# Optimization experiments

Measured on AMD Instinct MI355X. Metric: run time of the kernel, lower is better.

The kernel has to match this reference:

```python
import jax, jax.numpy as jnp
import numpy as np

B, N, E, D, AD = 2, 4096, 4, 64, 32


def setup_inputs() -> dict:
    key = jax.random.key(0)
    ks = jax.random.split(key, 10)
    s = 0.02  # init std matching module _initialization
    return {
        "prop_state": jax.random.normal(ks[0], (B, N, D), jnp.float32),
        "annotation": jax.random.normal(ks[1], (B, N, AD), jnp.float32),
        "A": jax.random.uniform(ks[2], (B, N, N * E), jnp.float32),
        "W_in": jax.random.normal(ks[3], (E, D, D), jnp.float32) * s,
        "b_in": jnp.zeros((E, D), jnp.float32),
        "Wr": jax.random.normal(ks[4], (D, 2 * D), jnp.float32) * s,
        "br": jnp.zeros((D,), jnp.float32),
        "Wz": jax.random.normal(ks[5], (D, 2 * D), jnp.float32) * s,
        "bz": jnp.zeros((D,), jnp.float32),
        "Wh": jax.random.normal(ks[6], (D, 2 * D), jnp.float32) * s,
        "bh": jnp.zeros((D,), jnp.float32),
        "Wo1": jax.random.normal(ks[7], (D, D + AD), jnp.float32) * s,
        "bo1": jnp.zeros((D,), jnp.float32),
        "Wo2": jax.random.normal(ks[8], (1, D), jnp.float32) * s,
        "bo2": jnp.zeros((1,), jnp.float32),
    }


def reference(prop_state, annotation, A, W_in, b_in, Wr, br, Wz, bz, Wh, bh, Wo1, bo1, Wo2, bo2):
    b, n, d = prop_state.shape
    e = W_in.shape[0]
    # per-edge-type input transforms: [B, E, N, D] -> [B, E*N, D] (edge-type major)
    in_states = jnp.einsum('bnd,eod->beno', prop_state, W_in) + b_in[None, :, None, :]
    in_flat = in_states.reshape(b, e * n, d)
    # dense adjacency aggregation: A [B, N, N*E] x in_flat [B, N*E, D]
    a_in = jnp.einsum('bnm,bmd->bnd', A, in_flat)
    # GRU-style gated node update
    a = jnp.concatenate([a_in, prop_state], axis=-1)  # [B, N, 2D]
    r = jax.nn.sigmoid(a @ Wr.T + br)
    z = jax.nn.sigmoid(a @ Wz.T + bz)
    h_hat = jnp.tanh(jnp.concatenate([a_in, r * prop_state], axis=-1) @ Wh.T + bh)
    new_state = (1.0 - z) * prop_state + z * h_hat  # [B, N, D]
    # output head
    join = jnp.concatenate([new_state, annotation], axis=-1)  # [B, N, D+AD]
    h = jnp.tanh(join @ Wo1.T + bo1)
    out = (h @ Wo2.T + bo2).sum(axis=2)  # [B, N]
    return out
```

## Files before the change

### kernel.cpp

```cpp
#include <hip/hip_runtime.h>
#include <hip/hip_bf16.h>
#include <stdint.h>

typedef __bf16 bf16x8 __attribute__((ext_vector_type(8)));
typedef float  f32x16 __attribute__((ext_vector_type(16)));
typedef float  f32x4  __attribute__((ext_vector_type(4)));

static constexpr int Bz = 2, Nn = 4096, Ee = 4, Dd = 64, ADim = 32;
static constexpr int Mm = Nn * Ee;
static constexpr int KSEG = 8;
static constexpr int KLEN = Mm / KSEG;
static constexpr int NT = Bz * Nn / 32;
static constexpr int PHK = 256;
static constexpr int NPH = KLEN / PHK;

__device__ __forceinline__ bf16x8 cvt8(float4 a, float4 b) {
  bf16x8 r;
  r[0] = (__bf16)a.x; r[1] = (__bf16)a.y; r[2] = (__bf16)a.z; r[3] = (__bf16)a.w;
  r[4] = (__bf16)b.x; r[5] = (__bf16)b.y; r[6] = (__bf16)b.z; r[7] = (__bf16)b.w;
  return r;
}
__device__ __forceinline__ bf16x8 cvt8v(f32x4 a, f32x4 b) {
  bf16x8 r;
  r[0] = (__bf16)a[0]; r[1] = (__bf16)a[1]; r[2] = (__bf16)a[2]; r[3] = (__bf16)a[3];
  r[4] = (__bf16)b[0]; r[5] = (__bf16)b[1]; r[6] = (__bf16)b[2]; r[7] = (__bf16)b[3];
  return r;
}
__device__ __forceinline__ f32x16 zero16() {
  f32x16 z;
#pragma unroll
  for (int i = 0; i < 16; ++i) z[i] = 0.f;
  return z;
}
__device__ __forceinline__ f32x16 mm(bf16x8 a, bf16x8 b, f32x16 c) {
  return __builtin_amdgcn_mfma_f32_32x32x16_bf16(a, b, c, 0, 0, 0);
}
__device__ __forceinline__ float sigm(float x) { return 1.f / (1.f + __expf(-x)); }
__device__ __forceinline__ float tanh_fast(float x) {
  float e = __expf(2.f * x);
  return 1.f - 2.f / (e + 1.f);
}
__device__ __forceinline__ void async_lds16(const void* g, void* l) {
  __builtin_amdgcn_global_load_lds(
      (const __attribute__((address_space(1))) uint32_t*)g,
      (__attribute__((address_space(3))) uint32_t*)l, 16, 0, 0);
}

__global__ __launch_bounds__(256) void k_packbt(
    const float* __restrict__ prop, const float* __restrict__ Win,
    const float* __restrict__ bin, __bf16* __restrict__ Bt,
    const float* __restrict__ Wr, const float* __restrict__ Wz,
    const float* __restrict__ Wh, const float* __restrict__ Wo1,
    __bf16* __restrict__ Wp) {
  const int bid = blockIdx.x;
  const int tid = threadIdx.x;
  const int w = tid >> 6, l = tid & 63;
  const int r31 = l & 31, h = l >> 5;

  if (bid == 512) {
    for (int f = w; f < 60; f += 4) {
      const float* W; int L, fl;
      if (f < 16)      { W = Wr;  L = 128; fl = f; }
      else if (f < 32) { W = Wz;  L = 128; fl = f - 16; }
      else if (f < 48) { W = Wh;  L = 128; fl = f - 32; }
      else             { W = Wo1; L = 96;  fl = f - 48; }
      const int ks = fl >> 1, oh = fl & 1;
      const float* src = W + (size_t)(32 * oh + r31) * L + 16 * ks + 8 * h;
      float4 s0 = *reinterpret_cast<const float4*>(src);
      float4 s1 = *reinterpret_cast<const float4*>(src + 4);
      *reinterpret_cast<bf16x8*>(Wp + ((size_t)f * 64 + l) * 8) = cvt8(s0, s1);
    }
    return;
  }
  const int nchunk = bid & 63;
  const int e = (bid >> 6) & 3, b = bid >> 8;
  const int oh = w & 1, ns = w >> 1;
  const int o_row = oh * 32 + r31;
  const int n_col = nchunk * 64 + ns * 32 + r31;
  const float* wbase = Win + ((size_t)e * 64 + o_row) * 64 + 8 * h;
  const float* pbase = prop + ((size_t)b * Nn + n_col) * 64 + 8 * h;
  f32x16 acc = zero16();
#pragma unroll
  for (int ks = 0; ks < 4; ++ks) {
    float4 w0 = *reinterpret_cast<const float4*>(wbase + 16 * ks);
    float4 w1 = *reinterpret_cast<const float4*>(wbase + 16 * ks + 4);
    float4 p0 = *reinterpret_cast<const float4*>(pbase + 16 * ks);
    float4 p1 = *reinterpret_cast<const float4*>(pbase + 16 * ks + 4);
    acc = mm(cvt8(w0, w1), cvt8(p0, p1), acc);
  }
#pragma unroll
  for (int reg = 0; reg < 16; ++reg) {
    int orow = oh * 32 + (reg & 3) + 8 * (reg >> 2) + 4 * h;
    float v = acc[reg] + bin[e * 64 + orow];
    Bt[((size_t)b * 64 + orow) * Mm + (size_t)e * Nn + n_col] = (__bf16)v;
  }
}

__global__ __launch_bounds__(512, 1) void k_big_gemm(
    const float* __restrict__ A, const __bf16* __restrict__ Bt,
    __bf16* __restrict__ part) {
  __shared__ float  ahalf[2][64][PHK];
  __shared__ __bf16 btl[64][PHK];

  const int bid = blockIdx.x;
  const int kseg = bid & 7;
  const int tg   = bid >> 3;
  const int bb   = tg >> 4;
  const int gg   = tg & 15;
  const int ph0  = tg & (NPH - 1);
  const int tid = threadIdx.x;
  const int w = tid >> 6, l = tid & 63;
  const int r31 = l & 31, h = l >> 5;
  const int tp = w >> 2, q = (w >> 1) & 1, kh = w & 1;

  const size_t kbase = (size_t)kseg * KLEN;
  const float*  Ab  = A  + ((size_t)bb * Nn + gg * 256) * Mm + kbase;
  const __bf16* BtB = Bt + (size_t)bb * 64 * Mm + kbase;

#define ISSUE_A(pi, pr, hf)                                                  \
  { _Pragma("unroll")                                                        \
    for (int j_ = 0; j_ < 8; ++j_) {                                         \
      const int rw_ = 8 * w + j_;                                            \
      const float* src_ = Ab + (size_t)((pi) * 64 + rw_) * Mm +              \
                          (size_t)(pr) * PHK + ((l ^ (rw_ & 7)) << 2);       \
      async_lds16(src_, (void*)&ahalf[hf][rw_][0]);                          \
    } }

  bf16x8 btreg[4];
  const int btrh = l >> 5;
  const int btu  = l & 31;
#define LOAD_BT(pr)                                                          \
  { _Pragma("unroll")                                                        \
    for (int j_ = 0; j_ < 4; ++j_) {                                         \
      const int row_ = 8 * w + 2 * j_ + btrh;                                \
      btreg[j_] = *reinterpret_cast<const bf16x8*>(                          \
          BtB + (size_t)row_ * Mm + (size_t)(pr) * PHK + btu * 8);           \
    } }
#define WRITE_BT                                                             \
  { _Pragma("unroll")                                                        \
    for (int j_ = 0; j_ < 4; ++j_) {                                         \
      const int row_ = 8 * w + 2 * j_ + btrh;                                \
      *reinterpret_cast<bf16x8*>(&btl[row_][(btu ^ (row_ & 7)) * 8]) =       \
          btreg[j_];                                                         \
    } }

  const int swz  = r31 & 7;
  const int arow = tp * 32 + r31;
  const int brow = 32 * q + r31;
  f32x16 acc[4] = {zero16(), zero16(), zero16(), zero16()};

#define COMPUTE(pi, hf)                                                      \
  { _Pragma("unroll")                                                        \
    for (int s_ = 0; s_ < 8; ++s_) {                                         \
      const int ua_ = kh * 32 + 4 * s_ + 2 * h;                              \
      f32x4 fa0 = *reinterpret_cast<const f32x4*>(                           \
          &ahalf[hf][arow][((ua_ ^ swz) << 2)]);                             \
      f32x4 fa1 = *reinterpret_cast<const f32x4*>(                           \
          &ahalf[hf][arow][(((ua_ + 1) ^ swz) << 2)]);                       \
      const int ub_ = kh * 16 + 2 * s_ + h;                                  \
      bf16x8 fb = *reinterpret_cast<const bf16x8*>(                          \
          &btl[brow][((ub_ ^ swz) * 8)]);                                    \
      acc[pi] = mm(cvt8v(fa0, fa1), fb, acc[pi]);                            \
    } }

  LOAD_BT(ph0);
  ISSUE_A(0, ph0, 0);
  ISSUE_A(1, ph0, 1);
  asm volatile("s_waitcnt vmcnt(16)" ::: "memory");
  WRITE_BT;
  asm volatile("s_waitcnt vmcnt(8) lgkmcnt(0)" ::: "memory");
  __builtin_amdgcn_s_barrier();

  for (int pp = 0; pp < NPH; ++pp) {
    const bool lastp = (pp == NPH - 1);
    const int prc = (pp + ph0) & (NPH - 1);
    const int prn = (pp + 1 + ph0) & (NPH - 1);
    COMPUTE(0, 0);
    __builtin_amdgcn_s_barrier();
    ISSUE_A(2, prc, 0);
    asm volatile("s_waitcnt vmcnt(8)" ::: "memory");
    __builtin_amdgcn_s_barrier();
    COMPUTE(1, 1);
    __builtin_amdgcn_s_barrier();
    if (!lastp) LOAD_BT(prn);
    ISSUE_A(3, prc, 1);
    asm volatile("s_waitcnt vmcnt(8)" ::: "memory");
    __builtin_amdgcn_s_barrier();
    COMPUTE(2, 0);
    __builtin_amdgcn_s_barrier();
    if (!lastp) {
      ISSUE_A(0, prn, 0);
      asm volatile("s_waitcnt vmcnt(8)" ::: "memory");
    } else {
      asm volatile("s_waitcnt vmcnt(0)" ::: "memory");
    }
    __builtin_amdgcn_s_barrier();
    COMPUTE(3, 1);
    if (!lastp) {
      __builtin_amdgcn_s_barrier();
      WRITE_BT;
      ISSUE_A(1, prn, 1);
      asm volatile("s_waitcnt vmcnt(8) lgkmcnt(0)" ::: "memory");
      __builtin_amdgcn_s_barrier();
    }
  }
#undef ISSUE_A
#undef LOAD_BT
#undef WRITE_BT
#undef COMPUTE

  float* scratch = &ahalf[0][0][0];
  if (kh == 1) {
#pragma unroll
    for (int i = 0; i < 4; ++i) {
      float* slot = scratch + (size_t)(i * 4 + tp * 2 + q) * 1024 + l * 16;
#pragma unroll
      for (int r = 0; r < 16; r += 4) {
        f32x4 v; v[0] = acc[i][r]; v[1] = acc[i][r + 1];
        v[2] = acc[i][r + 2]; v[3] = acc[i][r + 3];
        *reinterpret_cast<f32x4*>(slot + r) = v;
      }
    }
  }
  __syncthreads();
  if (kh == 0) {
#pragma unroll
    for (int i = 0; i < 4; ++i) {
      const int tile = bb * 128 + gg * 8 + i * 2 + tp;
      __bf16* pb = part + ((size_t)tile * KSEG + kseg) * 2048 + 32 * q;
      const float* slot = scratch + (size_t)(i * 4 + tp * 2 + q) * 1024 + l * 16;
#pragma unroll
      for (int reg = 0; reg < 16; ++reg) {
        int row = (reg & 3) + 8 * (reg >> 2) + 4 * h;
        pb[row * 64 + r31] = (__bf16)(acc[i][reg] + slot[reg]);
      }
    }
  }
}

__global__ __launch_bounds__(128) void k_gru(
    const __bf16* __restrict__ part, const float* __restrict__ prop,
    const float* __restrict__ annot, const __bf16* __restrict__ Wp,
    const float* __restrict__ br, const float* __restrict__ bz,
    const float* __restrict__ bh, const float* __restrict__ bo1,
    const float* __restrict__ Wo2, const float* __restrict__ bo2,
    float* __restrict__ out) {
  __shared__ float plds[32][68];
  __shared__ float tlds[32][68];
  __shared__ float sred[32];
  const int tile = blockIdx.x;
  const int R0 = tile * 32;
  const int tid = threadIdx.x;
  const int wv = tid >> 6;
  const int l = tid & 63;
  const int r31 = l & 31, h = l >> 5;

  bf16x8 xa[4], xp[4], xan[2];
  {
    const __bf16* pt = part + (size_t)tile * (KSEG * 2048) + (size_t)r31 * 64 + 8 * h;
    const float* pb = prop + (size_t)(R0 + r31) * 64 + 8 * h;
#pragma unroll
    for (int ks = 0; ks < 4; ++ks) {
      float s[8] = {0.f, 0.f, 0.f, 0.f, 0.f, 0.f, 0.f, 0.f};
#pragma unroll
      for (int seg = 0; seg < KSEG; ++seg) {
        bf16x8 v = *reinterpret_cast<const bf16x8*>(pt + seg * 2048 + 16 * ks);
#pragma unroll
        for (int j = 0; j < 8; ++j) s[j] += (float)v[j];
      }
      bf16x8 x;
#pragma unroll
      for (int j = 0; j < 8; ++j) x[j] = (__bf16)s[j];
      xa[ks] = x;
      float4 p0 = *reinterpret_cast<const float4*>(pb + 16 * ks);
      float4 p1 = *reinterpret_cast<const float4*>(pb + 16 * ks + 4);
      xp[ks] = cvt8(p0, p1);
      if (wv == 0) {
        *reinterpret_cast<float4*>(&plds[r31][16 * ks + 8 * h]) = p0;
        *reinterpret_cast<float4*>(&plds[r31][16 * ks + 8 * h + 4]) = p1;
      }
    }
    const float* anb = annot + (size_t)(R0 + r31) * ADim + 8 * h;
#pragma unroll
    for (int ks = 0; ks < 2; ++ks) {
      float4 a0 = *reinterpret_cast<const float4*>(anb + 16 * ks);
      float4 a1 = *reinterpret_cast<const float4*>(anb + 16 * ks + 4);
      xan[ks] = cvt8(a0, a1);
    }
  }
  __syncthreads();

#define LDWP(base, ks, oh) \
  (*reinterpret_cast<const bf16x8*>(Wp + (((size_t)(base) + (ks) * 2 + (oh)) * 64 + l) * 8))

  f32x16 aR = zero16(), aZ = zero16();
#pragma unroll
  for (int ks = 0; ks < 8; ++ks) {
    bf16x8 af = (ks < 4) ? xa[ks] : xp[ks - 4];
    aR = mm(af, LDWP(0, ks, wv), aR);
    aZ = mm(af, LDWP(16, ks, wv), aZ);
  }
  const float br_ = br[32 * wv + r31];
  const float bz_ = bz[32 * wv + r31];
  float propv[16], zv[16];
  const int oc = 32 * wv + r31;
#pragma unroll
  for (int reg = 0; reg < 16; ++reg) {
    int row = (reg & 3) + 8 * (reg >> 2) + 4 * h;
    propv[reg] = plds[row][oc];
    float rv = sigm(aR[reg] + br_);
    zv[reg] = sigm(aZ[reg] + bz_);
    tlds[row][oc] = rv * propv[reg];
  }
  __syncthreads();
  bf16x8 xr[4];
#pragma unroll
  for (int ks = 0; ks < 4; ++ks) {
    float4 t0 = *reinterpret_cast<const float4*>(&tlds[r31][16 * ks + 8 * h]);
    float4 t1 = *reinterpret_cast<const float4*>(&tlds[r31][16 * ks + 8 * h + 4]);
    xr[ks] = cvt8(t0, t1);
  }
  f32x16 aH = zero16();
#pragma unroll
  for (int ks = 0; ks < 8; ++ks) {
    bf16x8 af = (ks < 4) ? xa[ks] : xr[ks - 4];
    aH = mm(af, LDWP(32, ks, wv), aH);
  }
  __syncthreads();
  const float bh_ = bh[32 * wv + r31];
#pragma unroll
  for (int reg = 0; reg < 16; ++reg) {
    int row = (reg & 3) + 8 * (reg >> 2) + 4 * h;
    float hh = tanh_fast(aH[reg] + bh_);
    float z = zv[reg];
    tlds[row][oc] = (1.f - z) * propv[reg] + z * hh;
  }
  __syncthreads();
  bf16x8 xn[4];
#pragma unroll
  for (int ks = 0; ks < 4; ++ks) {
    float4 t0 = *reinterpret_cast<const float4*>(&tlds[r31][16 * ks + 8 * h]);
    float4 t1 = *reinterpret_cast<const float4*>(&tlds[r31][16 * ks + 8 * h + 4]);
    xn[ks] = cvt8(t0, t1);
  }
  f32x16 aO = zero16();
#pragma unroll
  for (int ks = 0; ks < 6; ++ks) {
    bf16x8 af = (ks < 4) ? xn[ks] : xan[ks - 4];
    aO = mm(af, LDWP(48, ks, wv), aO);
  }
  const float bo1_ = bo1[32 * wv + r31];
  const float wo2_ = Wo2[32 * wv + r31];
  const float bo2v = bo2[0];
  float pred[16];
#pragma unroll
  for (int reg = 0; reg < 16; ++reg) {
    float p = tanh_fast(aO[reg] + bo1_) * wo2_;
#pragma unroll
    for (int mks = 16; mks >= 1; mks >>= 1) p += __shfl_xor(p, mks, 64);
    pred[reg] = p;
  }
  if (wv == 1 && r31 == 0) {
#pragma unroll
    for (int reg = 0; reg < 16; ++reg) sred[reg * 2 + h] = pred[reg];
  }
  __syncthreads();
  if (wv == 0 && r31 == 0) {
#pragma unroll
    for (int reg = 0; reg < 16; ++reg) {
      int row = (reg & 3) + 8 * (reg >> 2) + 4 * h;
      out[R0 + row] = pred[reg] + sred[reg * 2 + h] + bo2v;
    }
  }
#undef LDWP
}

extern "C" void kernel_launch(void* const* d_in, const int* in_sizes, int n_in,
                              void* d_out, int out_size, void* d_ws, size_t ws_size,
                              hipStream_t stream) {
  const float* prop  = (const float*)d_in[0];
  const float* annot = (const float*)d_in[1];
  const float* A     = (const float*)d_in[2];
  const float* Win   = (const float*)d_in[3];
  const float* bin   = (const float*)d_in[4];
  const float* Wr    = (const float*)d_in[5];
  const float* br    = (const float*)d_in[6];
  const float* Wz    = (const float*)d_in[7];
  const float* bz    = (const float*)d_in[8];
  const float* Wh    = (const float*)d_in[9];
  const float* bh    = (const float*)d_in[10];
  const float* Wo1   = (const float*)d_in[11];
  const float* bo1   = (const float*)d_in[12];
  const float* Wo2   = (const float*)d_in[13];
  const float* bo2   = (const float*)d_in[14];
  float* out = (float*)d_out;

  char* ws = (char*)d_ws;
  __bf16* Bt   = (__bf16*)ws;
  __bf16* part = (__bf16*)(ws + (size_t)4 * 1024 * 1024);
  __bf16* Wp   = (__bf16*)(ws + (size_t)16 * 1024 * 1024);

  k_packbt<<<dim3(513), 256, 0, stream>>>(prop, Win, bin, Bt,
                                          Wr, Wz, Wh, Wo1, Wp);
  k_big_gemm<<<dim3(256), 512, 0, stream>>>(A, Bt, part);
  k_gru<<<dim3(NT), 128, 0, stream>>>(part, prop, annot, Wp,
                                      br, bz, bh, bo1, Wo2, bo2, out);
}
```

Before: 127.8 us.

## Fuse pack, big GEMM and GRU kernels into one cooperative kernel

Merges the three launches (B-transpose pack, split-K adjacency GEMM, GRU/output head) into a single cooperative kernel of 256 blocks separated by grid-wide syncs. Shared memory is unioned between the GEMM and GRU phases, and the pack work is remapped so each 512-thread block covers two of the old 256-thread blocks. The aim is to remove the launch gaps and tail effects between kernels. The cost is two grid barriers, and in the GRU phase only 2 of 8 waves do work, leaving 256 blocks of mostly idle threads.

```diff
diff --git a/kernel.cpp b/kernel.cpp
--- a/kernel.cpp
+++ b/kernel.cpp
@@ -1,6 +1,9 @@
 #include <hip/hip_runtime.h>
 #include <hip/hip_bf16.h>
+#include <hip/hip_cooperative_groups.h>
 #include <stdint.h>
+
+namespace cg = cooperative_groups;
 
 typedef __bf16 bf16x8 __attribute__((ext_vector_type(8)));
 typedef float  f32x16 __attribute__((ext_vector_type(16)));
@@ -46,76 +49,82 @@
       (__attribute__((address_space(3))) uint32_t*)l, 16, 0, 0);
 }
 
-__global__ __launch_bounds__(256) void k_packbt(
-    const float* __restrict__ prop, const float* __restrict__ Win,
-    const float* __restrict__ bin, __bf16* __restrict__ Bt,
-    const float* __restrict__ Wr, const float* __restrict__ Wz,
-    const float* __restrict__ Wh, const float* __restrict__ Wo1,
-    __bf16* __restrict__ Wp) {
+__global__ __launch_bounds__(512, 1) void k_fused(
+    const float* __restrict__ prop, const float* __restrict__ annot,
+    const float* __restrict__ A, const float* __restrict__ Win,
+    const float* __restrict__ bin,
+    const float* __restrict__ Wr, const float* __restrict__ br,
+    const float* __restrict__ Wz, const float* __restrict__ bz,
+    const float* __restrict__ Wh, const float* __restrict__ bh,
+    const float* __restrict__ Wo1, const float* __restrict__ bo1,
+    const float* __restrict__ Wo2, const float* __restrict__ bo2,
+    __bf16* __restrict__ Bt, __bf16* __restrict__ part,
+    __bf16* __restrict__ Wp, float* __restrict__ out) {
+  __shared__ union {
+    struct { float ahalf[2][64][PHK]; __bf16 btl[64][PHK]; } g;
+    struct { float plds[32][68]; float tlds[32][68]; float sred[32]; } r;
+  } smem;
+
+  cg::grid_group grid = cg::this_grid();
   const int bid = blockIdx.x;
   const int tid = threadIdx.x;
   const int w = tid >> 6, l = tid & 63;
   const int r31 = l & 31, h = l >> 5;
 
-  if (bid == 512) {
-    for (int f = w; f < 60; f += 4) {
-      const float* W; int L, fl;
-      if (f < 16)      { W = Wr;  L = 128; fl = f; }
-      else if (f < 32) { W = Wz;  L = 128; fl = f - 16; }
-      else if (f < 48) { W = Wh;  L = 128; fl = f - 32; }
-      else             { W = Wo1; L = 96;  fl = f - 48; }
-      const int ks = fl >> 1, oh = fl & 1;
-      const float* src = W + (size_t)(32 * oh + r31) * L + 16 * ks + 8 * h;
-      float4 s0 = *reinterpret_cast<const float4*>(src);
-      float4 s1 = *reinterpret_cast<const float4*>(src + 4);
-      *reinterpret_cast<bf16x8*>(Wp + ((size_t)f * 64 + l) * 8) = cvt8(s0, s1);
-    }
-    return;
+  {
+    const int sub = 2 * bid + (w >> 2);
+    const int wsub = w & 3;
+    const int nchunk = sub & 63;
+    const int e = (sub >> 6) & 3, b = sub >> 8;
+    const int oh = wsub & 1, ns = wsub >> 1;
+    const int o_row = oh * 32 + r31;
+    const int n_col = nchunk * 64 + ns * 32 + r31;
+    const float* wbase = Win + ((size_t)e * 64 + o_row) * 64 + 8 * h;
+    const float* pbase = prop + ((size_t)b * Nn + n_col) * 64 + 8 * h;
+    f32x16 acc = zero16();
+#pragma unroll
+    for (int ks = 0; ks < 4; ++ks) {
+      float4 w0 = *reinterpret_cast<const float4*>(wbase + 16 * ks);
+      float4 w1 = *reinterpret_cast<const float4*>(wbase + 16 * ks + 4);
+      float4 p0 = *reinterpret_cast<const float4*>(pbase + 16 * ks);
+      float4 p1 = *reinterpret_cast<const float4*>(pbase + 16 * ks + 4);
+      acc = mm(cvt8(w0, w1), cvt8(p0, p1), acc);
+    }
+#pragma unroll
+    for (int reg = 0; reg < 16; ++reg) {
+      int orow = oh * 32 + (reg & 3) + 8 * (reg >> 2) + 4 * h;
+      float v = acc[reg] + bin[e * 64 + orow];
+      Bt[((size_t)b * 64 + orow) * Mm + (size_t)e * Nn + n_col] = (__bf16)v;
+    }
+    if (bid == 0) {
+      for (int f = w; f < 60; f += 8) {
+        const float* W; int L, fl;
+        if (f < 16)      { W = Wr;  L = 128; fl = f; }
+        else if (f < 32) { W = Wz;  L = 128; fl = f - 16; }
+        else if (f < 48) { W = Wh;  L = 128; fl = f - 32; }
+        else             { W = Wo1; L = 96;  fl = f - 48; }
+        const int ks = fl >> 1, oh2 = fl & 1;
+        const float* src = W + (size_t)(32 * oh2 + r31) * L + 16 * ks + 8 * h;
+        float4 s0 = *reinterpret_cast<const float4*>(src);
+        float4 s1 = *reinterpret_cast<const float4*>(src + 4);
+        *reinterpret_cast<bf16x8*>(Wp + ((size_t)f * 64 + l) * 8) = cvt8(s0, s1);
+      }
+    }
   }
-  const int nchunk = bid & 63;
-  const int e = (bid >> 6) & 3, b = bid >> 8;
-  const int oh = w & 1, ns = w >> 1;
-  const int o_row = oh * 32 + r31;
-  const int n_col = nchunk * 64 + ns * 32 + r31;
-  const float* wbase = Win + ((size_t)e * 64 + o_row) * 64 + 8 * h;
-  const float* pbase = prop + ((size_t)b * Nn + n_col) * 64 + 8 * h;
-  f32x16 acc = zero16();
-#pragma unroll
-  for (int ks = 0; ks < 4; ++ks) {
-    float4 w0 = *reinterpret_cast<const float4*>(wbase + 16 * ks);
-    float4 w1 = *reinterpret_cast<const float4*>(wbase + 16 * ks + 4);
-    float4 p0 = *reinterpret_cast<const float4*>(pbase + 16 * ks);
-    float4 p1 = *reinterpret_cast<const float4*>(pbase + 16 * ks + 4);
-    acc = mm(cvt8(w0, w1), cvt8(p0, p1), acc);
-  }
-#pragma unroll
-  for (int reg = 0; reg < 16; ++reg) {
-    int orow = oh * 32 + (reg & 3) + 8 * (reg >> 2) + 4 * h;
-    float v = acc[reg] + bin[e * 64 + orow];
-    Bt[((size_t)b * 64 + orow) * Mm + (size_t)e * Nn + n_col] = (__bf16)v;
-  }
-}
-
-__global__ __launch_bounds__(512, 1) void k_big_gemm(
-    const float* __restrict__ A, const __bf16* __restrict__ Bt,
-    __bf16* __restrict__ part) {
-  __shared__ float  ahalf[2][64][PHK];
-  __shared__ __bf16 btl[64][PHK];
-
-  const int bid = blockIdx.x;
-  const int kseg = bid & 7;
-  const int tg   = bid >> 3;
-  const int bb   = tg >> 4;
-  const int gg   = tg & 15;
-  const int ph0  = tg & (NPH - 1);
-  const int tid = threadIdx.x;
-  const int w = tid >> 6, l = tid & 63;
-  const int r31 = l & 31, h = l >> 5;
-  const int tp = w >> 2, q = (w >> 1) & 1, kh = w & 1;
-
-  const size_t kbase = (size_t)kseg * KLEN;
-  const float*  Ab  = A  + ((size_t)bb * Nn + gg * 256) * Mm + kbase;
-  const __bf16* BtB = Bt + (size_t)bb * 64 * Mm + kbase;
+  __threadfence();
+  grid.sync();
+
+  {
+    const int kseg = bid & 7;
+    const int tg   = bid >> 3;
+    const int bb   = tg >> 4;
+    const int gg   = tg & 15;
+    const int ph0  = tg & (NPH - 1);
+    const int tp = w >> 2, q = (w >> 1) & 1, kh = w & 1;
+
+    const size_t kbase = (size_t)kseg * KLEN;
+    const float*  Ab  = A  + ((size_t)bb * Nn + gg * 256) * Mm + kbase;
+    const __bf16* BtB = Bt + (size_t)bb * 64 * Mm + kbase;
 
 #define ISSUE_A(pi, pr, hf)                                                  \
   { _Pragma("unroll")                                                        \
@@ -123,12 +132,12 @@
       const int rw_ = 8 * w + j_;                                            \
       const float* src_ = Ab + (size_t)((pi) * 64 + rw_) * Mm +              \
                           (size_t)(pr) * PHK + ((l ^ (rw_ & 7)) << 2);       \
-      async_lds16(src_, (void*)&ahalf[hf][rw_][0]);                          \
+      async_lds16(src_, (void*)&smem.g.ahalf[hf][rw_][0]);                   \
     } }
 
-  bf16x8 btreg[4];
-  const int btrh = l >> 5;
-  const int btu  = l & 31;
+    bf16x8 btreg[4];
+    const int btrh = l >> 5;
+    const int btu  = l & 31;
 #define LOAD_BT(pr)                                                          \
   { _Pragma("unroll")                                                        \
     for (int j_ = 0; j_ < 4; ++j_) {                                         \
@@ -140,239 +149,233 @@
   { _Pragma("unroll")                                                        \
     for (int j_ = 0; j_ < 4; ++j_) {                                         \
       const int row_ = 8 * w + 2 * j_ + btrh;                                \
-      *reinterpret_cast<bf16x8*>(&btl[row_][(btu ^ (row_ & 7)) * 8]) =       \
-          btreg[j_];                                                         \
+      *reinterpret_cast<bf16x8*>(&smem.g.btl[row_][(btu ^ (row_ & 7)) * 8])  \
+          = btreg[j_];                                                       \
     } }
 
-  const int swz  = r31 & 7;
-  const int arow = tp * 32 + r31;
-  const int brow = 32 * q + r31;
-  f32x16 acc[4] = {zero16(), zero16(), zero16(), zero16()};
+    const int swz  = r31 & 7;
+    const int arow = tp * 32 + r31;
+    const int brow = 32 * q + r31;
+    f32x16 acc[4] = {zero16(), zero16(), zero16(), zero16()};
 
 #define COMPUTE(pi, hf)                                                      \
   { _Pragma("unroll")                                                        \
     for (int s_ = 0; s_ < 8; ++s_) {                                         \
       const int ua_ = kh * 32 + 4 * s_ + 2 * h;                              \
       f32x4 fa0 = *reinterpret_cast<const f32x4*>(                           \
-          &ahalf[hf][arow][((ua_ ^ swz) << 2)]);                             \
+          &smem.g.ahalf[hf][arow][((ua_ ^ swz) << 2)]);                      \
       f32x4 fa1 = *reinterpret_cast<const f32x4*>(                           \
-          &ahalf[hf][arow][(((ua_ + 1) ^ swz) << 2)]);                       \
+          &smem.g.ahalf[hf][arow][(((ua_ + 1) ^ swz) << 2)]);                \
       const int ub_ = kh * 16 + 2 * s_ + h;                                  \
       bf16x8 fb = *reinterpret_cast<const bf16x8*>(                          \
-          &btl[brow][((ub_ ^ swz) * 8)]);                                    \
+          &smem.g.btl[brow][((ub_ ^ swz) * 8)]);                             \
       acc[pi] = mm(cvt8v(fa0, fa1), fb, acc[pi]);                            \
     } }
 
-  LOAD_BT(ph0);
-  ISSUE_A(0, ph0, 0);
-  ISSUE_A(1, ph0, 1);
-  asm volatile("s_waitcnt vmcnt(16)" ::: "memory");
-  WRITE_BT;
-  asm volatile("s_waitcnt vmcnt(8) lgkmcnt(0)" ::: "memory");
-  __builtin_amdgcn_s_barrier();
-
-  for (int pp = 0; pp < NPH; ++pp) {
-    const bool lastp = (pp == NPH - 1);
-    const int prc = (pp + ph0) & (NPH - 1);
-    const int prn = (pp + 1 + ph0) & (NPH - 1);
-    COMPUTE(0, 0);
+    LOAD_BT(ph0);
+    ISSUE_A(0, ph0, 0);
+    ISSUE_A(1, ph0, 1);
+    asm volatile("s_waitcnt vmcnt(16)" ::: "memory");
+    WRITE_BT;
+    asm volatile("s_waitcnt vmcnt(8) lgkmcnt(0)" ::: "memory");
     __builtin_amdgcn_s_barrier();
-    ISSUE_A(2, prc, 0);
-    asm volatile("s_waitcnt vmcnt(8)" ::: "memory");
-    __builtin_amdgcn_s_barrier();
-    COMPUTE(1, 1);
-    __builtin_amdgcn_s_barrier();
-    if (!lastp) LOAD_BT(prn);
-    ISSUE_A(3, prc, 1);
-    asm volatile("s_waitcnt vmcnt(8)" ::: "memory");
-    __builtin_amdgcn_s_barrier();
-    COMPUTE(2, 0);
-    __builtin_amdgcn_s_barrier();
-    if (!lastp) {
-      ISSUE_A(0, prn, 0);
+
+    for (int pp = 0; pp < NPH; ++pp) {
+      const bool lastp = (pp == NPH - 1);
+      const int prc = (pp + ph0) & (NPH - 1);
+      const int prn = (pp + 1 + ph0) & (NPH - 1);
+      COMPUTE(0, 0);
+      __builtin_amdgcn_s_barrier();
+      ISSUE_A(2, prc, 0);
       asm volatile("s_waitcnt vmcnt(8)" ::: "memory");
-    } else {
-      asm volatile("s_waitcnt vmcnt(0)" ::: "memory");
-    }
-    __builtin_amdgcn_s_barrier();
-    COMPUTE(3, 1);
-    if (!lastp) {
-      __builtin_amdgcn_s_barrier();
-      WRITE_BT;
-      ISSUE_A(1, prn, 1);
-      asm volatile("s_waitcnt vmcnt(8) lgkmcnt(0)" ::: "memory");
-      __builtin_amdgcn_s_barrier();
-    }
-  }
+      __builtin_amdgcn_s_barrier();
+      COMPUTE(1, 1);
+      __builtin_amdgcn_s_barrier();
+      if (!lastp) LOAD_BT(prn);
+      ISSUE_A(3, prc, 1);
+      asm volatile("s_waitcnt vmcnt(8)" ::: "memory");
+      __builtin_amdgcn_s_barrier();
+      COMPUTE(2, 0);
+      __builtin_amdgcn_s_barrier();
+      if (!lastp) {
+        ISSUE_A(0, prn, 0);
+        asm volatile("s_waitcnt vmcnt(8)" ::: "memory");
+      } else {
+        asm volatile("s_waitcnt vmcnt(0)" ::: "memory");
+      }
+      __builtin_amdgcn_s_barrier();
+      COMPUTE(3, 1);
+      if (!lastp) {
+        __builtin_amdgcn_s_barrier();
+        WRITE_BT;
+        ISSUE_A(1, prn, 1);
+        asm volatile("s_waitcnt vmcnt(8) lgkmcnt(0)" ::: "memory");
+        __builtin_amdgcn_s_barrier();
+      }
+    }
 #undef ISSUE_A
 #undef LOAD_BT
 #undef WRITE_BT
 #undef COMPUTE
 
-  float* scratch = &ahalf[0][0][0];
-  if (kh == 1) {
-#pragma unroll
-    for (int i = 0; i < 4; ++i) {
-      float* slot = scratch + (size_t)(i * 4 + tp * 2 + q) * 1024 + l * 16;
-#pragma unroll
-      for (int r = 0; r < 16; r += 4) {
-        f32x4 v; v[0] = acc[i][r]; v[1] = acc[i][r + 1];
-        v[2] = acc[i][r + 2]; v[3] = acc[i][r + 3];
-        *reinterpret_cast<f32x4*>(slot + r) = v;
+    float* scratch = &smem.g.ahalf[0][0][0];
+    if (kh == 1) {
+#pragma unroll
+      for (int i = 0; i < 4; ++i) {
+        float* slot = scratch + (size_t)(i * 4 + tp * 2 + q) * 1024 + l * 16;
+#pragma unroll
+        for (int r = 0; r < 16; r += 4) {
+          f32x4 v; v[0] = acc[i][r]; v[1] = acc[i][r + 1];
+          v[2] = acc[i][r + 2]; v[3] = acc[i][r + 3];
+          *reinterpret_cast<f32x4*>(slot + r) = v;
+        }
+      }
+    }
+    __syncthreads();
+    if (kh == 0) {
+#pragma unroll
+      for (int i = 0; i < 4; ++i) {
+        const int tile = bb * 128 + gg * 8 + i * 2 + tp;
+        __bf16* pb = part + ((size_t)tile * KSEG + kseg) * 2048 + 32 * q;
+        const float* slot = scratch + (size_t)(i * 4 + tp * 2 + q) * 1024 + l * 16;
+#pragma unroll
+        for (int reg = 0; reg < 16; ++reg) {
+          int row = (reg & 3) + 8 * (reg >> 2) + 4 * h;
+          pb[row * 64 + r31] = (__bf16)(acc[i][reg] + slot[reg]);
+        }
       }
     }
   }
-  __syncthreads();
-  if (kh == 0) {
-#pragma unroll
-    for (int i = 0; i < 4; ++i) {
-      const int tile = bb * 128 + gg * 8 + i * 2 + tp;
-      __bf16* pb = part + ((size_t)tile * KSEG + kseg) * 2048 + 32 * q;
-      const float* slot = scratch + (size_t)(i * 4 + tp * 2 + q) * 1024 + l * 16;
+  __threadfence();
+  grid.sync();
+
+  {
+    const int tile = bid;
+    const int R0 = tile * 32;
+    const int wv = w;
+    const int wk = wv & 1;
+    bf16x8 xa[4], xp[4], xan[2], xr[4], xn[4];
+    float propv[16], zv[16], pred[16];
+    f32x16 aR = zero16(), aZ = zero16(), aH = zero16(), aO = zero16();
+    const int oc = 32 * wk + r31;
+
+#define LDWP(base, ks, oh) \
+  (*reinterpret_cast<const bf16x8*>(Wp + (((size_t)(base) + (ks) * 2 + (oh)) * 64 + l) * 8))
+
+    if (wv < 2) {
+      const __bf16* pt = part + (size_t)tile * (KSEG * 2048) + (size_t)r31 * 64 + 8 * h;
+      const float* pb = prop + (size_t)(R0 + r31) * 64 + 8 * h;
+#pragma unroll
+      for (int ks = 0; ks < 4; ++ks) {
+        float s[8] = {0.f, 0.f, 0.f, 0.f, 0.f, 0.f, 0.f, 0.f};
+#pragma unroll
+        for (int seg = 0; seg < KSEG; ++seg) {
+          bf16x8 v = *reinterpret_cast<const bf16x8*>(pt + seg * 2048 + 16 * ks);
+#pragma unroll
+          for (int j = 0; j < 8; ++j) s[j] += (float)v[j];
+        }
+        bf16x8 x;
+#pragma unroll
+        for (int j = 0; j < 8; ++j) x[j] = (__bf16)s[j];
+        xa[ks] = x;
+        float4 p0 = *reinterpret_cast<const float4*>(pb + 16 * ks);
+        float4 p1 = *reinterpret_cast<const float4*>(pb + 16 * ks + 4);
+        xp[ks] = cvt8(p0, p1);
+        if (wv == 0) {
+          *reinterpret_cast<float4*>(&smem.r.plds[r31][16 * ks + 8 * h]) = p0;
+          *reinterpret_cast<float4*>(&smem.r.plds[r31][16 * ks + 8 * h + 4]) = p1;
+        }
+      }
+      const float* anb = annot + (size_t)(R0 + r31) * ADim + 8 * h;
+#pragma unroll
+      for (int ks = 0; ks < 2; ++ks) {
+        float4 a0 = *reinterpret_cast<const float4*>(anb + 16 * ks);
+        float4 a1 = *reinterpret_cast<const float4*>(anb + 16 * ks + 4);
+        xan[ks] = cvt8(a0, a1);
+      }
+    }
+    __syncthreads();
+    if (wv < 2) {
+#pragma unroll
+      for (int ks = 0; ks < 8; ++ks) {
+        bf16x8 af = (ks < 4) ? xa[ks] : xp[ks - 4];
+        aR = mm(af, LDWP(0, ks, wk), aR);
+        aZ = mm(af, LDWP(16, ks, wk), aZ);
+      }
+      const float br_ = br[32 * wk + r31];
+      const float bz_ = bz[32 * wk + r31];
 #pragma unroll
       for (int reg = 0; reg < 16; ++reg) {
         int row = (reg & 3) + 8 * (reg >> 2) + 4 * h;
-        pb[row * 64 + r31] = (__bf16)(acc[i][reg] + slot[reg]);
-      }
-    }
+        propv[reg] = smem.r.plds[row][oc];
+        float rv = sigm(aR[reg] + br_);
+        zv[reg] = sigm(aZ[reg] + bz_);
+        smem.r.tlds[row][oc] = rv * propv[reg];
+      }
+    }
+    __syncthreads();
+    if (wv < 2) {
+#pragma unroll
+      for (int ks = 0; ks < 4; ++ks) {
+        float4 t0 = *reinterpret_cast<const float4*>(&smem.r.tlds[r31][16 * ks + 8 * h]);
+        float4 t1 = *reinterpret_cast<const float4*>(&smem.r.tlds[r31][16 * ks + 8 * h + 4]);
+        xr[ks] = cvt8(t0, t1);
+      }
+#pragma unroll
+      for (int ks = 0; ks < 8; ++ks) {
+        bf16x8 af = (ks < 4) ? xa[ks] : xr[ks - 4];
+        aH = mm(af, LDWP(32, ks, wk), aH);
+      }
+    }
+    __syncthreads();
+    if (wv < 2) {
+      const float bh_ = bh[32 * wk + r31];
+#pragma unroll
+      for (int reg = 0; reg < 16; ++reg) {
+        int row = (reg & 3) + 8 * (reg >> 2) + 4 * h;
+        float hh = tanh_fast(aH[reg] + bh_);
+        float z = zv[reg];
+        smem.r.tlds[row][oc] = (1.f - z) * propv[reg] + z * hh;
+      }
+    }
+    __syncthreads();
+    if (wv < 2) {
+#pragma unroll
+      for (int ks = 0; ks < 4; ++ks) {
+        float4 t0 = *reinterpret_cast<const float4*>(&smem.r.tlds[r31][16 * ks + 8 * h]);
+        float4 t1 = *reinterpret_cast<const float4*>(&smem.r.tlds[r31][16 * ks + 8 * h + 4]);
+        xn[ks] = cvt8(t0, t1);
+      }
+#pragma unroll
+      for (int ks = 0; ks < 6; ++ks) {
+        bf16x8 af = (ks < 4) ? xn[ks] : xan[ks - 4];
+        aO = mm(af, LDWP(48, ks, wk), aO);
+      }
+      const float bo1_ = bo1[32 * wk + r31];
+      const float wo2_ = Wo2[32 * wk + r31];
+#pragma unroll
+      for (int reg = 0; reg < 16; ++reg) {
+        float p = tanh_fast(aO[reg] + bo1_) * wo2_;
+#pragma unroll
+        for (int mks = 16; mks >= 1; mks >>= 1) p += __shfl_xor(p, mks, 64);
+        pred[reg] = p;
+      }
+      if (wv == 1 && r31 == 0) {
+#pragma unroll
+        for (int reg = 0; reg < 16; ++reg) smem.r.sred[reg * 2 + h] = pred[reg];
+      }
+    }
+    __syncthreads();
+    if (wv == 0 && r31 == 0) {
+      const float bo2v = bo2[0];
+#pragma unroll
+      for (int reg = 0; reg < 16; ++reg) {
+        int row = (reg & 3) + 8 * (reg >> 2) + 4 * h;
+        out[R0 + row] = pred[reg] + smem.r.sred[reg * 2 + h] + bo2v;
+      }
+    }
+#undef LDWP
   }
-}
-
-__global__ __launch_bounds__(128) void k_gru(
-    const __bf16* __restrict__ part, const float* __restrict__ prop,
-    const float* __restrict__ annot, const __bf16* __restrict__ Wp,
-    const float* __restrict__ br, const float* __restrict__ bz,
-    const float* __restrict__ bh, const float* __restrict__ bo1,
-    const float* __restrict__ Wo2, const float* __restrict__ bo2,
-    float* __restrict__ out) {
-  __shared__ float plds[32][68];
-  __shared__ float tlds[32][68];
-  __shared__ float sred[32];
-  const int tile = blockIdx.x;
-  const int R0 = tile * 32;
-  const int tid = threadIdx.x;
-  const int wv = tid >> 6;
-  const int l = tid & 63;
-  const int r31 = l & 31, h = l >> 5;
-
-  bf16x8 xa[4], xp[4], xan[2];
-  {
-    const __bf16* pt = part + (size_t)tile * (KSEG * 2048) + (size_t)r31 * 64 + 8 * h;
-    const float* pb = prop + (size_t)(R0 + r31) * 64 + 8 * h;
-#pragma unroll
-    for (int ks = 0; ks < 4; ++ks) {
-      float s[8] = {0.f, 0.f, 0.f, 0.f, 0.f, 0.f, 0.f, 0.f};
-#pragma unroll
-      for (int seg = 0; seg < KSEG; ++seg) {
-        bf16x8 v = *reinterpret_cast<const bf16x8*>(pt + seg * 2048 + 16 * ks);
-#pragma unroll
-        for (int j = 0; j < 8; ++j) s[j] += (float)v[j];
-      }
-      bf16x8 x;
-#pragma unroll
-      for (int j = 0; j < 8; ++j) x[j] = (__bf16)s[j];
-      xa[ks] = x;
-      float4 p0 = *reinterpret_cast<const float4*>(pb + 16 * ks);
-      float4 p1 = *reinterpret_cast<const float4*>(pb + 16 * ks + 4);
-      xp[ks] = cvt8(p0, p1);
-      if (wv == 0) {
-        *reinterpret_cast<float4*>(&plds[r31][16 * ks + 8 * h]) = p0;
-        *reinterpret_cast<float4*>(&plds[r31][16 * ks + 8 * h + 4]) = p1;
-      }
-    }
-    const float* anb = annot + (size_t)(R0 + r31) * ADim + 8 * h;
-#pragma unroll
-    for (int ks = 0; ks < 2; ++ks) {
-      float4 a0 = *reinterpret_cast<const float4*>(anb + 16 * ks);
-      float4 a1 = *reinterpret_cast<const float4*>(anb + 16 * ks + 4);
-      xan[ks] = cvt8(a0, a1);
-    }
-  }
-  __syncthreads();
-
-#define LDWP(base, ks, oh) \
-  (*reinterpret_cast<const bf16x8*>(Wp + (((size_t)(base) + (ks) * 2 + (oh)) * 64 + l) * 8))
-
-  f32x16 aR = zero16(), aZ = zero16();
-#pragma unroll
-  for (int ks = 0; ks < 8; ++ks) {
-    bf16x8 af = (ks < 4) ? xa[ks] : xp[ks - 4];
-    aR = mm(af, LDWP(0, ks, wv), aR);
-    aZ = mm(af, LDWP(16, ks, wv), aZ);
-  }
-  const float br_ = br[32 * wv + r31];
-  const float bz_ = bz[32 * wv + r31];
-  float propv[16], zv[16];
-  const int oc = 32 * wv + r31;
-#pragma unroll
-  for (int reg = 0; reg < 16; ++reg) {
-    int row = (reg & 3) + 8 * (reg >> 2) + 4 * h;
-    propv[reg] = plds[row][oc];
-    float rv = sigm(aR[reg] + br_);
-    zv[reg] = sigm(aZ[reg] + bz_);
-    tlds[row][oc] = rv * propv[reg];
-  }
-  __syncthreads();
-  bf16x8 xr[4];
-#pragma unroll
-  for (int ks = 0; ks < 4; ++ks) {
-    float4 t0 = *reinterpret_cast<const float4*>(&tlds[r31][16 * ks + 8 * h]);
-    float4 t1 = *reinterpret_cast<const float4*>(&tlds[r31][16 * ks + 8 * h + 4]);
-    xr[ks] = cvt8(t0, t1);
-  }
-  f32x16 aH = zero16();
-#pragma unroll
-  for (int ks = 0; ks < 8; ++ks) {
-    bf16x8 af = (ks < 4) ? xa[ks] : xr[ks - 4];
-    aH = mm(af, LDWP(32, ks, wv), aH);
-  }
-  __syncthreads();
-  const float bh_ = bh[32 * wv + r31];
-#pragma unroll
-  for (int reg = 0; reg < 16; ++reg) {
-    int row = (reg & 3) + 8 * (reg >> 2) + 4 * h;
-    float hh = tanh_fast(aH[reg] + bh_);
-    float z = zv[reg];
-    tlds[row][oc] = (1.f - z) * propv[reg] + z * hh;
-  }
-  __syncthreads();
-  bf16x8 xn[4];
-#pragma unroll
-  for (int ks = 0; ks < 4; ++ks) {
-    float4 t0 = *reinterpret_cast<const float4*>(&tlds[r31][16 * ks + 8 * h]);
-    float4 t1 = *reinterpret_cast<const float4*>(&tlds[r31][16 * ks + 8 * h + 4]);
-    xn[ks] = cvt8(t0, t1);
-  }
-  f32x16 aO = zero16();
-#pragma unroll
-  for (int ks = 0; ks < 6; ++ks) {
-    bf16x8 af = (ks < 4) ? xn[ks] : xan[ks - 4];
-    aO = mm(af, LDWP(48, ks, wv), aO);
-  }
-  const float bo1_ = bo1[32 * wv + r31];
-  const float wo2_ = Wo2[32 * wv + r31];
-  const float bo2v = bo2[0];
-  float pred[16];
-#pragma unroll
-  for (int reg = 0; reg < 16; ++reg) {
-    float p = tanh_fast(aO[reg] + bo1_) * wo2_;
-#pragma unroll
-    for (int mks = 16; mks >= 1; mks >>= 1) p += __shfl_xor(p, mks, 64);
-    pred[reg] = p;
-  }
-  if (wv == 1 && r31 == 0) {
-#pragma unroll
-    for (int reg = 0; reg < 16; ++reg) sred[reg * 2 + h] = pred[reg];
-  }
-  __syncthreads();
-  if (wv == 0 && r31 == 0) {
-#pragma unroll
-    for (int reg = 0; reg < 16; ++reg) {
-      int row = (reg & 3) + 8 * (reg >> 2) + 4 * h;
-      out[R0 + row] = pred[reg] + sred[reg * 2 + h] + bo2v;
-    }
-  }
-#undef LDWP
 }
 
 extern "C" void kernel_launch(void* const* d_in, const int* in_sizes, int n_in,
@@ -400,9 +403,11 @@
   __bf16* part = (__bf16*)(ws + (size_t)4 * 1024 * 1024);
   __bf16* Wp   = (__bf16*)(ws + (size_t)16 * 1024 * 1024);
 
-  k_packbt<<<dim3(513), 256, 0, stream>>>(prop, Win, bin, Bt,
-                                          Wr, Wz, Wh, Wo1, Wp);
-  k_big_gemm<<<dim3(256), 512, 0, stream>>>(A, Bt, part);
-  k_gru<<<dim3(NT), 128, 0, stream>>>(part, prop, annot, Wp,
-                                      br, bz, bh, bo1, Wo2, bo2, out);
-}
+  void* args[] = {
+      (void*)&prop, (void*)&annot, (void*)&A, (void*)&Win, (void*)&bin,
+      (void*)&Wr, (void*)&br, (void*)&Wz, (void*)&bz, (void*)&Wh, (void*)&bh,
+      (void*)&Wo1, (void*)&bo1, (void*)&Wo2, (void*)&bo2,
+      (void*)&Bt, (void*)&part, (void*)&Wp, (void*)&out};
+  hipLaunchCooperativeKernel((const void*)k_fused, dim3(256), dim3(512),
+                             args, 0, stream);
+}
```

New measurement: 335.3 us. +162.4%, slower.
